# Kernel optimization log

Measured on AMD Instinct MI355X. Metric: run time of the kernel, lower is better.

## Reference

```python
import jax, jax.numpy as jnp
import numpy as np

R = 6
P = 2 * R + 1          # 13, correlation patch size
N = P * P              # 169 displacements
C = 32                 # one-hot label channels
FOUR_LN2 = 4.0 * float(np.log(2.0))


def _extract_windows(x, h, w):
    """Zero-pad by R and extract all PxP shifted views.
    x: (b, c, h, w) -> (b, c, N, h, w), displacement index n = dy*P + dx,
    matching both SpatialCorrelationSampler patch ordering and F.unfold."""
    xp = jnp.pad(x, ((0, 0), (0, 0), (R, R), (R, R)))
    return jnp.stack([xp[:, :, dy:dy + h, dx:dx + w]
                      for dy in range(P) for dx in range(P)], axis=2)


def setup_inputs():
    key = jax.random.key(0)
    k1, k2, k3 = jax.random.split(key, 3)
    feats_r = jax.random.normal(k1, (2, 2, 128, 64, 64), dtype=jnp.float32)
    feats_t = jax.random.normal(k2, (2, 128, 64, 64), dtype=jnp.float32)
    quantized_r = jax.random.randint(k3, (2, 2, 1, 256, 256), 0, C)
    return {"feats_r": feats_r, "feats_t": feats_t, "quantized_r": quantized_r}


def reference(feats_r, feats_t, quantized_r):
    nref, b, c, h, w = feats_r.shape
    hw = h * w

    # ---- local PxP correlation volume per reference (SpatialCorrelationSampler, k=1) ----
    corrs = []
    for i in range(nref):
        win = _extract_windows(feats_r[i], h, w)                       # (b,c,N,h,w)
        corrs.append(jnp.einsum('bchw,bcnhw->bnhw', feats_t, win).reshape(b, N, hw))
    corr = jax.nn.softmax(jnp.concatenate(corrs, axis=1), axis=1)      # (b, nref*N, hw)

    # ---- compact_verify: top-2 + gaussian heatmap refinement ----
    cc = corr.reshape(b, nref, N, hw).transpose(0, 1, 3, 2).reshape(b, nref * hw, N)
    ccd = jax.lax.stop_gradient(cc)                                     # torch uses .detach()
    vals, idx = jax.lax.top_k(ccd, 2)                                   # (b, L, 2)
    wts = jax.nn.softmax(vals, axis=-1)
    ys = (idx // P).astype(jnp.float32)
    xs = (idx % P).astype(jnp.float32)
    grid = jnp.arange(P, dtype=jnp.float32)
    dx = grid[None, None, None, :] - xs[..., None]                      # (b,L,2,P)
    dy = grid[None, None, None, :] - ys[..., None]                      # (b,L,2,P)
    heat = jnp.exp(-FOUR_LN2 * (dx[:, :, :, None, :] ** 2 + dy[:, :, :, :, None] ** 2))  # (b,L,2,P,P) [yy,xx]
    corr_heat = jnp.einsum('blkn,blk->bln', heat.reshape(b, nref * hw, 2, N), wts)
    vmax = jnp.max(vals, axis=-1, keepdims=True)
    corr2 = jnp.where(vmax > 0.1, corr_heat, cc)                        # mask/refine
    corr2 = corr2.reshape(b, nref, hw, N).transpose(0, 1, 3, 2).reshape(b, nref * N, hw)

    # ---- get_out: unfold one-hot reference labels and weighted-sum over window ----
    scale = quantized_r.shape[-2] // h                                  # prep: stride subsample
    ufs = []
    for i in range(nref):
        lab = quantized_r[i, :, 0, ::scale, ::scale]                    # (b,h,w)
        oh = jnp.transpose(jax.nn.one_hot(lab, C, dtype=feats_t.dtype), (0, 3, 1, 2))
        ufs.append(_extract_windows(oh, h, w).reshape(b, C, N, hw))
    image_uf = jnp.concatenate(ufs, axis=2)                             # (b,C,nref*N,hw)
    image_uf = image_uf.at[:, 1:].multiply(1.15)                        # inference boost
    out = jnp.einsum('bnl,bcnl->bcl', corr2, image_uf)
    return out.reshape(b, C, h, w)
```

## Files before the change

### kernel.cpp

```cpp
#include <hip/hip_runtime.h>
#include <math.h>

namespace {

constexpr int RAD  = 6;
constexpr int P    = 13;
constexpr int NWIN = 169;
constexpr int NTOT = 338;
constexpr int NCH  = 128;
constexpr int NCLS = 32;
constexpr int W    = 64;
constexpr int HW   = 4096;
constexpr float FOUR_LN2 = 2.772588722239781f;

constexpr int TX    = 32;
constexpr int CHUNK = 8;
constexpr int PW    = 48;
constexpr int PR    = 13;
constexpr int FRELEMS = CHUNK * PR * PW;
constexpr int NLD   = 20;
constexpr int NCHUNK = NCH / CHUNK;
constexpr int TILE  = TX * NWIN;
constexpr size_t VOLF = (size_t)2 * HW * NTOT;

__device__ __forceinline__ bool better(float va, int ia, float vb, int ib) {
  return (va > vb) || ((va == vb) && (ia < ib));
}

__global__ __launch_bounds__(256, 2) void corr_kernel(
    const float* __restrict__ fr,
    const float* __restrict__ ft,
    float* __restrict__ vol,
    const int* __restrict__ q,
    int* __restrict__ lab) {
  const int blk = blockIdx.x;
  const int t  = threadIdx.x;

  if (blk < 64) {
    const int idx = blk * 256 + t;
    const int i2b = idx >> 12;
    const int rem = idx & 4095;
    const int y2  = rem >> 6;
    const int x2  = rem & 63;
    lab[idx] = q[(size_t)i2b * 65536 + (y2 * 4) * 256 + x2 * 4];
  }

  const int lb = (blk & 7) * 64 + (blk >> 3);
  const int xh = lb & 1;
  const int y  = (lb >> 1) & 63;
  const int bi = lb >> 7;
  const int b  = bi >> 1;
  const int ii = bi & 1;
  const int x0 = xh * TX;
  const int cg = t >> 7;
  const int tl = t & 127;

  __shared__ __align__(16) float smem[2 * FRELEMS];
  __shared__ __align__(16) float ftbuf[2][CHUNK * TX];

  const int xg = tl & 7;
  const int dy = tl >> 3;
  const bool comp = (tl < 104);

  const float* frbase = fr + (size_t)((ii * 2 + b) * NCH) * HW;
  const float* ftp = ft + (size_t)(b * NCH + (t >> 5)) * HW + y * W + x0 + (t & 31);

  int offc[NLD];
  unsigned vmsk = 0u;
  #pragma unroll
  for (int u = 0; u < NLD; ++u) {
    const int e = t + u * 256;
    int o = 0;
    if (e < FRELEMS) {
      const int cc  = e / (PR * PW);
      const int rem = e - cc * (PR * PW);
      const int r   = rem / PW;
      const int xc  = rem - r * PW;
      const int yy  = y + r - RAD;
      const int xx  = x0 - RAD + xc;
      if ((unsigned)yy < 64u && (unsigned)xx < 64u && xc < 44) {
        o = cc * HW + yy * W + xx;
        vmsk |= (1u << u);
      }
    }
    offc[u] = o;
  }

  float acc[13][4];
  #pragma unroll
  for (int dx = 0; dx < 13; ++dx)
    #pragma unroll
    for (int k = 0; k < 4; ++k) acc[dx][k] = 0.f;

  float rg[NLD];
  float rft;

  auto stage_load = [&](int c0) {
    const float* fb = frbase + (size_t)c0 * HW;
    #pragma unroll
    for (int u = 0; u < NLD; ++u) {
      const float v = fb[offc[u]];
      rg[u] = (vmsk & (1u << u)) ? v : 0.f;
    }
    rft = ftp[(size_t)c0 * HW];
  };
  auto stage_write = [&](int s) {
    float* frb = smem + s * FRELEMS;
    #pragma unroll
    for (int u = 0; u < NLD; ++u) {
      const int e = t + u * 256;
      if (e < FRELEMS) frb[e] = rg[u];
    }
    ftbuf[s][t] = rft;
  };

  stage_load(0);
  stage_write(0);
  __syncthreads();

  for (int k = 0; k < NCHUNK; ++k) {
    const int cur = k & 1;
    if (k < NCHUNK - 1) stage_load((k + 1) * CHUNK);
    if (comp) {
      const float* frb = smem + cur * FRELEMS;
      #pragma unroll
      for (int c2 = 0; c2 < 4; ++c2) {
        const int cc = cg * 4 + c2;
        const float* fp = frb + (cc * PR + dy) * PW + xg * 4;
        float w[16];
        #pragma unroll
        for (int j = 0; j < 4; ++j) {
          const float4 q4 = *(const float4*)(fp + 4 * j);
          w[4 * j] = q4.x; w[4 * j + 1] = q4.y; w[4 * j + 2] = q4.z; w[4 * j + 3] = q4.w;
        }
        const float4 tq = *(const float4*)(&ftbuf[cur][cc * TX + xg * 4]);
        const float tqa[4] = {tq.x, tq.y, tq.z, tq.w};
        #pragma unroll
        for (int dx = 0; dx < 13; ++dx)
          #pragma unroll
          for (int kk = 0; kk < 4; ++kk)
            acc[dx][kk] = fmaf(w[dx + kk], tqa[kk], acc[dx][kk]);
      }
    }
    if (k < NCHUNK - 1) stage_write(cur ^ 1);
    __syncthreads();
  }

  if (comp && cg == 1) {
    float* rb = smem + tl * 52;
    #pragma unroll
    for (int dx = 0; dx < 13; ++dx)
      *(float4*)(rb + dx * 4) = make_float4(acc[dx][0], acc[dx][1], acc[dx][2], acc[dx][3]);
  }
  __syncthreads();
  if (comp && cg == 0) {
    const float* rb = smem + tl * 52;
    #pragma unroll
    for (int dx = 0; dx < 13; ++dx) {
      const float4 r = *(const float4*)(rb + dx * 4);
      acc[dx][0] += r.x; acc[dx][1] += r.y; acc[dx][2] += r.z; acc[dx][3] += r.w;
    }
  }
  __syncthreads();
  if (comp && cg == 0) {
    #pragma unroll
    for (int dx = 0; dx < 13; ++dx)
      #pragma unroll
      for (int kk = 0; kk < 4; ++kk)
        smem[(xg * 4 + kk) * NWIN + dy * 13 + dx] = acc[dx][kk];
  }
  __syncthreads();
  {
    float* gb = vol + ((size_t)(b * HW + y * W + x0) * 2 + ii) * NWIN;
    for (int u = 0; u < 22; ++u) {
      const int e = t + u * 256;
      if (e < TILE) {
        const int xl2 = e / NWIN;
        const int mm  = e - xl2 * NWIN;
        gb[(size_t)xl2 * (2 * NWIN) + mm] = smem[e];
      }
    }
  }
}

__global__ __launch_bounds__(256) void post_kernel(
    const float* __restrict__ vol,
    const int*  __restrict__ lab,
    float* __restrict__ out) {
  const int blk  = blockIdx.x;
  const int t    = threadIdx.x;
  const int w    = t >> 6;
  const int lane = t & 63;
  const int pix  = blk * 4 + w;
  const int b = pix >> 12;
  const int y = (pix >> 6) & 63;
  const int x = pix & 63;

  __shared__ float accS[4][NCLS];
  accS[w][lane & 31] = 0.f;

  float vv[6];
  float lmax = -INFINITY;
  const float* vp = vol + (size_t)pix * NTOT;
  #pragma unroll
  for (int k = 0; k < 6; ++k) {
    const int e = lane + 64 * k;
    vv[k] = (e < NTOT) ? vp[e] : -INFINITY;
    lmax = fmaxf(lmax, vv[k]);
  }
  #pragma unroll
  for (int off = 32; off > 0; off >>= 1)
    lmax = fmaxf(lmax, __shfl_xor(lmax, off));

  float p[6];
  float lsum = 0.f;
  #pragma unroll
  for (int k = 0; k < 6; ++k) {
    const int e = lane + 64 * k;
    p[k] = (e < NTOT) ? __expf(vv[k] - lmax) : 0.f;
    lsum += p[k];
  }
  #pragma unroll
  for (int off = 32; off > 0; off >>= 1)
    lsum += __shfl_xor(lsum, off);
  const float rinv = 1.f / lsum;
  #pragma unroll
  for (int k = 0; k < 6; ++k) p[k] *= rinv;

  float a1_0 = -1.f, a2_0 = -1.f, a1_1 = -1.f, a2_1 = -1.f;
  int   j1_0 = 1 << 20, j2_0 = 1 << 20, j1_1 = 1 << 20, j2_1 = 1 << 20;
  #pragma unroll
  for (int k = 0; k < 6; ++k) {
    const int e = lane + 64 * k;
    if (e < NTOT) {
      const int r = (e >= NWIN) ? 1 : 0;
      const int m = e - r * NWIN;
      const float pv = p[k];
      if (r == 0) {
        if (better(pv, m, a1_0, j1_0)) { a2_0 = a1_0; j2_0 = j1_0; a1_0 = pv; j1_0 = m; }
        else if (better(pv, m, a2_0, j2_0)) { a2_0 = pv; j2_0 = m; }
      } else {
        if (better(pv, m, a1_1, j1_1)) { a2_1 = a1_1; j2_1 = j1_1; a1_1 = pv; j1_1 = m; }
        else if (better(pv, m, a2_1, j2_1)) { a2_1 = pv; j2_1 = m; }
      }
    }
  }
  #pragma unroll
  for (int off = 32; off > 0; off >>= 1) {
    {
      const float u1 = __shfl_xor(a1_0, off); const int q1 = __shfl_xor(j1_0, off);
      const float u2 = __shfl_xor(a2_0, off); const int q2 = __shfl_xor(j2_0, off);
      if (better(u1, q1, a1_0, j1_0)) {
        float nv2; int ni2;
        if (better(a1_0, j1_0, u2, q2)) { nv2 = a1_0; ni2 = j1_0; }
        else                            { nv2 = u2;   ni2 = q2; }
        a1_0 = u1; j1_0 = q1; a2_0 = nv2; j2_0 = ni2;
      } else if (better(u1, q1, a2_0, j2_0)) { a2_0 = u1; j2_0 = q1; }
    }
    {
      const float u1 = __shfl_xor(a1_1, off); const int q1 = __shfl_xor(j1_1, off);
      const float u2 = __shfl_xor(a2_1, off); const int q2 = __shfl_xor(j2_1, off);
      if (better(u1, q1, a1_1, j1_1)) {
        float nv2; int ni2;
        if (better(a1_1, j1_1, u2, q2)) { nv2 = a1_1; ni2 = j1_1; }
        else                            { nv2 = u2;   ni2 = q2; }
        a1_1 = u1; j1_1 = q1; a2_1 = nv2; j2_1 = ni2;
      } else if (better(u1, q1, a2_1, j2_1)) { a2_1 = u1; j2_1 = q1; }
    }
  }

  const float e10 = __expf(a1_0), e20 = __expf(a2_0);
  const float rs0 = 1.f / (e10 + e20);
  const float w00 = e10 * rs0, w10 = e20 * rs0;
  const bool  fl0 = (a1_0 > 0.1f);
  const float xs00 = (float)(j1_0 % P), ys00 = (float)(j1_0 / P);
  const float xs10 = (float)(j2_0 % P), ys10 = (float)(j2_0 / P);

  const float e11 = __expf(a1_1), e21 = __expf(a2_1);
  const float rs1 = 1.f / (e11 + e21);
  const float w01 = e11 * rs1, w11 = e21 * rs1;
  const bool  fl1 = (a1_1 > 0.1f);
  const float xs01 = (float)(j1_1 % P), ys01 = (float)(j1_1 / P);
  const float xs11 = (float)(j2_1 % P), ys11 = (float)(j2_1 / P);

  #pragma unroll
  for (int k = 0; k < 6; ++k) {
    const int e = lane + 64 * k;
    if (e < NTOT) {
      const int r  = (e >= NWIN) ? 1 : 0;
      const int m  = e - r * NWIN;
      const int dy = m / P;
      const int dx = m - dy * P;
      const bool  fl = r ? fl1 : fl0;
      float val;
      if (fl) {
        const float wA = r ? w01 : w00, wB = r ? w11 : w10;
        const float xA = r ? xs01 : xs00, yA = r ? ys01 : ys00;
        const float xB = r ? xs11 : xs10, yB = r ? ys11 : ys10;
        const float fdx0 = (float)dx - xA, fdy0 = (float)dy - yA;
        const float fdx1 = (float)dx - xB, fdy1 = (float)dy - yB;
        val = wA * __expf(-FOUR_LN2 * (fdx0 * fdx0 + fdy0 * fdy0))
            + wB * __expf(-FOUR_LN2 * (fdx1 * fdx1 + fdy1 * fdy1));
      } else {
        val = p[k];
      }
      const int yy = y + dy - RAD;
      const int xx = x + dx - RAD;
      if ((unsigned)yy < 64u && (unsigned)xx < 64u) {
        const int cls = lab[(size_t)(r * 2 + b) * 4096 + yy * W + xx];
        atomicAdd(&accS[w][cls], val);
      }
    }
  }
  __syncthreads();

  if (t < 4 * NCLS) {
    const int cls = t >> 2;
    const int j   = t & 3;
    const int x0  = (blk * 4) & 63;
    const float sc = (cls == 0) ? 1.0f : 1.15f;
    out[(size_t)(b * NCLS + cls) * HW + y * W + x0 + j] = accS[j][cls] * sc;
  }
}

}

extern "C" void kernel_launch(void* const* d_in, const int* in_sizes, int n_in,
                              void* d_out, int out_size, void* d_ws, size_t ws_size,
                              hipStream_t stream) {
  const float* fr = (const float*)d_in[0];
  const float* ft = (const float*)d_in[1];
  const int*   q  = (const int*)d_in[2];
  float* out = (float*)d_out;
  float* vol = (float*)d_ws;
  int*   lab = (int*)((char*)d_ws + VOLF * sizeof(float));

  corr_kernel<<<dim3(2 * 2 * 64 * 2), dim3(256), 0, stream>>>(fr, ft, vol, q, lab);
  post_kernel<<<dim3(2 * HW / 4), dim3(256), 0, stream>>>(vol, lab, out);
}
```

Before: 58.77 us.

## Split correlation blocks by displacement-row halves to double grid and occupancy

Each correlation block now handles only 7 or 6 of the 13 vertical displacement rows, which doubles the grid to 2048 blocks and roughly halves shared memory and per-thread accumulators. Threads now compute 2 pixels × 13 dx instead of 4 × 13, and launch bounds are raised to allow 4 blocks per CU. The aim is more parallelism and better latency hiding on a grid that was small. The cost is that feats_t is loaded twice, reference rows overlap partly between halves, and fewer FMAs are done per shared-memory load.

Measured after the change: 59.16 us. About the same (+0.7%).

```diff
diff --git a/kernel.cpp b/kernel.cpp
--- a/kernel.cpp
+++ b/kernel.cpp
@@ -16,18 +16,16 @@
 constexpr int TX    = 32;
 constexpr int CHUNK = 8;
 constexpr int PW    = 48;
-constexpr int PR    = 13;
-constexpr int FRELEMS = CHUNK * PR * PW;
-constexpr int NLD   = 20;
+constexpr int FRMAX = CHUNK * 7 * PW;
+constexpr int NLD   = 11;
 constexpr int NCHUNK = NCH / CHUNK;
-constexpr int TILE  = TX * NWIN;
 constexpr size_t VOLF = (size_t)2 * HW * NTOT;
 
 __device__ __forceinline__ bool better(float va, int ia, float vb, int ib) {
   return (va > vb) || ((va == vb) && (ia < ib));
 }
 
-__global__ __launch_bounds__(256, 2) void corr_kernel(
+__global__ __launch_bounds__(256, 4) void corr_kernel(
     const float* __restrict__ fr,
     const float* __restrict__ ft,
     float* __restrict__ vol,
@@ -45,22 +43,29 @@
     lab[idx] = q[(size_t)i2b * 65536 + (y2 * 4) * 256 + x2 * 4];
   }
 
-  const int lb = (blk & 7) * 64 + (blk >> 3);
-  const int xh = lb & 1;
-  const int y  = (lb >> 1) & 63;
-  const int bi = lb >> 7;
+  const int lb = (blk & 7) * 128 + (blk >> 3);
+  const int h  = lb & 1;
+  const int xh = (lb >> 1) & 1;
+  const int y  = (lb >> 2) & 63;
+  const int bi = lb >> 8;
   const int b  = bi >> 1;
   const int ii = bi & 1;
   const int x0 = xh * TX;
   const int cg = t >> 7;
   const int tl = t & 127;
 
-  __shared__ __align__(16) float smem[2 * FRELEMS];
+  const int RH    = 7 - h;
+  const int yb    = h ? (y + 1) : (y - 6);
+  const int m0    = h * 91;
+  const int frele = CHUNK * RH * PW;
+  const int msz   = RH * P;
+
+  __shared__ __align__(16) float smem[2 * FRMAX];
   __shared__ __align__(16) float ftbuf[2][CHUNK * TX];
 
-  const int xg = tl & 7;
-  const int dy = tl >> 3;
-  const bool comp = (tl < 104);
+  const int xp  = tl & 15;
+  const int dyl = tl >> 4;
+  const bool comp = (dyl < RH);
 
   const float* frbase = fr + (size_t)((ii * 2 + b) * NCH) * HW;
   const float* ftp = ft + (size_t)(b * NCH + (t >> 5)) * HW + y * W + x0 + (t & 31);
@@ -71,12 +76,12 @@
   for (int u = 0; u < NLD; ++u) {
     const int e = t + u * 256;
     int o = 0;
-    if (e < FRELEMS) {
-      const int cc  = e / (PR * PW);
-      const int rem = e - cc * (PR * PW);
+    if (e < frele) {
+      const int cc  = e / (RH * PW);
+      const int rem = e - cc * (RH * PW);
       const int r   = rem / PW;
       const int xc  = rem - r * PW;
-      const int yy  = y + r - RAD;
+      const int yy  = yb + r;
       const int xx  = x0 - RAD + xc;
       if ((unsigned)yy < 64u && (unsigned)xx < 64u && xc < 44) {
         o = cc * HW + yy * W + xx;
@@ -86,11 +91,9 @@
     offc[u] = o;
   }
 
-  float acc[13][4];
-  #pragma unroll
-  for (int dx = 0; dx < 13; ++dx)
-    #pragma unroll
-    for (int k = 0; k < 4; ++k) acc[dx][k] = 0.f;
+  float acc[13][2];
+  #pragma unroll
+  for (int dx = 0; dx < 13; ++dx) { acc[dx][0] = 0.f; acc[dx][1] = 0.f; }
 
   float rg[NLD];
   float rft;
@@ -105,11 +108,11 @@
     rft = ftp[(size_t)c0 * HW];
   };
   auto stage_write = [&](int s) {
-    float* frb = smem + s * FRELEMS;
+    float* frb = smem + s * FRMAX;
     #pragma unroll
     for (int u = 0; u < NLD; ++u) {
       const int e = t + u * 256;
-      if (e < FRELEMS) frb[e] = rg[u];
+      if (e < frele) frb[e] = rg[u];
     }
     ftbuf[s][t] = rft;
   };
@@ -122,24 +125,20 @@
     const int cur = k & 1;
     if (k < NCHUNK - 1) stage_load((k + 1) * CHUNK);
     if (comp) {
-      const float* frb = smem + cur * FRELEMS;
+      const float* frb = smem + cur * FRMAX;
       #pragma unroll
       for (int c2 = 0; c2 < 4; ++c2) {
         const int cc = cg * 4 + c2;
-        const float* fp = frb + (cc * PR + dy) * PW + xg * 4;
-        float w[16];
+        const float* fp = frb + (cc * RH + dyl) * PW + xp * 2;
+        float w[14];
         #pragma unroll
-        for (int j = 0; j < 4; ++j) {
-          const float4 q4 = *(const float4*)(fp + 4 * j);
-          w[4 * j] = q4.x; w[4 * j + 1] = q4.y; w[4 * j + 2] = q4.z; w[4 * j + 3] = q4.w;
+        for (int j = 0; j < 14; ++j) w[j] = fp[j];
+        const float2 tq = *(const float2*)(&ftbuf[cur][cc * TX + xp * 2]);
+        #pragma unroll
+        for (int dx = 0; dx < 13; ++dx) {
+          acc[dx][0] = fmaf(w[dx    ], tq.x, acc[dx][0]);
+          acc[dx][1] = fmaf(w[dx + 1], tq.y, acc[dx][1]);
         }
-        const float4 tq = *(const float4*)(&ftbuf[cur][cc * TX + xg * 4]);
-        const float tqa[4] = {tq.x, tq.y, tq.z, tq.w};
-        #pragma unroll
-        for (int dx = 0; dx < 13; ++dx)
-          #pragma unroll
-          for (int kk = 0; kk < 4; ++kk)
-            acc[dx][kk] = fmaf(w[dx + kk], tqa[kk], acc[dx][kk]);
       }
     }
     if (k < NCHUNK - 1) stage_write(cur ^ 1);
@@ -147,38 +146,38 @@
   }
 
   if (comp && cg == 1) {
-    float* rb = smem + tl * 52;
-    #pragma unroll
-    for (int dx = 0; dx < 13; ++dx)
-      *(float4*)(rb + dx * 4) = make_float4(acc[dx][0], acc[dx][1], acc[dx][2], acc[dx][3]);
+    float* rb = smem + tl * 26;
+    #pragma unroll
+    for (int dx = 0; dx < 13; ++dx) {
+      rb[dx * 2]     = acc[dx][0];
+      rb[dx * 2 + 1] = acc[dx][1];
+    }
   }
   __syncthreads();
   if (comp && cg == 0) {
-    const float* rb = smem + tl * 52;
+    const float* rb = smem + tl * 26;
     #pragma unroll
     for (int dx = 0; dx < 13; ++dx) {
-      const float4 r = *(const float4*)(rb + dx * 4);
-      acc[dx][0] += r.x; acc[dx][1] += r.y; acc[dx][2] += r.z; acc[dx][3] += r.w;
+      acc[dx][0] += rb[dx * 2];
+      acc[dx][1] += rb[dx * 2 + 1];
     }
   }
   __syncthreads();
   if (comp && cg == 0) {
     #pragma unroll
-    for (int dx = 0; dx < 13; ++dx)
-      #pragma unroll
-      for (int kk = 0; kk < 4; ++kk)
-        smem[(xg * 4 + kk) * NWIN + dy * 13 + dx] = acc[dx][kk];
+    for (int dx = 0; dx < 13; ++dx) {
+      smem[(xp * 2    ) * msz + dyl * P + dx] = acc[dx][0];
+      smem[(xp * 2 + 1) * msz + dyl * P + dx] = acc[dx][1];
+    }
   }
   __syncthreads();
   {
-    float* gb = vol + ((size_t)(b * HW + y * W + x0) * 2 + ii) * NWIN;
-    for (int u = 0; u < 22; ++u) {
-      const int e = t + u * 256;
-      if (e < TILE) {
-        const int xl2 = e / NWIN;
-        const int mm  = e - xl2 * NWIN;
-        gb[(size_t)xl2 * (2 * NWIN) + mm] = smem[e];
-      }
+    const int tot = TX * msz;
+    float* gb = vol + ((size_t)(b * HW + y * W + x0) * 2 + ii) * NWIN + m0;
+    for (int e = t; e < tot; e += 256) {
+      const int px = e / msz;
+      const int m  = e - px * msz;
+      gb[(size_t)px * (2 * NWIN) + m] = smem[e];
     }
   }
 }
@@ -335,6 +334,6 @@
   float* vol = (float*)d_ws;
   int*   lab = (int*)((char*)d_ws + VOLF * sizeof(float));
 
-  corr_kernel<<<dim3(2 * 2 * 64 * 2), dim3(256), 0, stream>>>(fr, ft, vol, q, lab);
+  corr_kernel<<<dim3(2 * 2 * 64 * 2 * 2), dim3(256), 0, stream>>>(fr, ft, vol, q, lab);
   post_kernel<<<dim3(2 * HW / 4), dim3(256), 0, stream>>>(vol, lab, out);
 }
```

## Widen correlation register tile to 8 pixels per thread and pack load offsets

Applied to the files above, without the earlier changes.

Each compute thread now accumulates 8 output pixels across all 13 horizontal displacements instead of 4, so only 52 of every 128 threads compute. This raises FMA reuse per shared-memory load. Load offsets are packed two per 32-bit register, and out-of-range loads are skipped outright, with shared memory zeroed once up front instead of writing zeros every stage. This cuts register pressure and memory traffic, but it halves the active compute threads and roughly doubles the accumulator registers, which can hurt latency hiding.

Result: slower. 197.9 us (+236.8%).

```diff
diff --git a/kernel.cpp b/kernel.cpp
--- a/kernel.cpp
+++ b/kernel.cpp
@@ -58,19 +58,19 @@
   __shared__ __align__(16) float smem[2 * FRELEMS];
   __shared__ __align__(16) float ftbuf[2][CHUNK * TX];
 
-  const int xg = tl & 7;
-  const int dy = tl >> 3;
-  const bool comp = (tl < 104);
+  const int xg = tl & 3;
+  const int dy = tl >> 2;
+  const bool comp = (tl < 52);
 
   const float* frbase = fr + (size_t)((ii * 2 + b) * NCH) * HW;
   const float* ftp = ft + (size_t)(b * NCH + (t >> 5)) * HW + y * W + x0 + (t & 31);
 
-  int offc[NLD];
+  unsigned offp[10];
   unsigned vmsk = 0u;
   #pragma unroll
   for (int u = 0; u < NLD; ++u) {
     const int e = t + u * 256;
-    int o = 0;
+    unsigned o = 0;
     if (e < FRELEMS) {
       const int cc  = e / (PR * PW);
       const int rem = e - cc * (PR * PW);
@@ -79,18 +79,20 @@
       const int yy  = y + r - RAD;
       const int xx  = x0 - RAD + xc;
       if ((unsigned)yy < 64u && (unsigned)xx < 64u && xc < 44) {
-        o = cc * HW + yy * W + xx;
+        o = (unsigned)(cc * HW + yy * W + xx);
         vmsk |= (1u << u);
       }
     }
-    offc[u] = o;
-  }
-
-  float acc[13][4];
+    if (u & 1) offp[u >> 1] |= (o << 16); else offp[u >> 1] = o;
+  }
+
+  for (int e = t; e < 2 * FRELEMS; e += 256) smem[e] = 0.f;
+
+  float acc[13][8];
   #pragma unroll
   for (int dx = 0; dx < 13; ++dx)
     #pragma unroll
-    for (int k = 0; k < 4; ++k) acc[dx][k] = 0.f;
+    for (int px = 0; px < 8; ++px) acc[dx][px] = 0.f;
 
   float rg[NLD];
   float rft;
@@ -99,18 +101,18 @@
     const float* fb = frbase + (size_t)c0 * HW;
     #pragma unroll
     for (int u = 0; u < NLD; ++u) {
-      const float v = fb[offc[u]];
-      rg[u] = (vmsk & (1u << u)) ? v : 0.f;
+      if (vmsk & (1u << u)) {
+        const int o = (u & 1) ? (int)(offp[u >> 1] >> 16) : (int)(offp[u >> 1] & 0xffffu);
+        rg[u] = fb[o];
+      }
     }
     rft = ftp[(size_t)c0 * HW];
   };
   auto stage_write = [&](int s) {
     float* frb = smem + s * FRELEMS;
     #pragma unroll
-    for (int u = 0; u < NLD; ++u) {
-      const int e = t + u * 256;
-      if (e < FRELEMS) frb[e] = rg[u];
-    }
+    for (int u = 0; u < NLD; ++u)
+      if (vmsk & (1u << u)) frb[t + u * 256] = rg[u];
     ftbuf[s][t] = rft;
   };
 
@@ -126,20 +128,21 @@
       #pragma unroll
       for (int c2 = 0; c2 < 4; ++c2) {
         const int cc = cg * 4 + c2;
-        const float* fp = frb + (cc * PR + dy) * PW + xg * 4;
-        float w[16];
+        const float* fp = frb + (cc * PR + dy) * PW + xg * 8;
+        float w[20];
         #pragma unroll
-        for (int j = 0; j < 4; ++j) {
+        for (int j = 0; j < 5; ++j) {
           const float4 q4 = *(const float4*)(fp + 4 * j);
           w[4 * j] = q4.x; w[4 * j + 1] = q4.y; w[4 * j + 2] = q4.z; w[4 * j + 3] = q4.w;
         }
-        const float4 tq = *(const float4*)(&ftbuf[cur][cc * TX + xg * 4]);
-        const float tqa[4] = {tq.x, tq.y, tq.z, tq.w};
+        const float4 ta = *(const float4*)(&ftbuf[cur][cc * TX + xg * 8]);
+        const float4 tb = *(const float4*)(&ftbuf[cur][cc * TX + xg * 8 + 4]);
+        const float tq8[8] = {ta.x, ta.y, ta.z, ta.w, tb.x, tb.y, tb.z, tb.w};
         #pragma unroll
         for (int dx = 0; dx < 13; ++dx)
           #pragma unroll
-          for (int kk = 0; kk < 4; ++kk)
-            acc[dx][kk] = fmaf(w[dx + kk], tqa[kk], acc[dx][kk]);
+          for (int px = 0; px < 8; ++px)
+            acc[dx][px] = fmaf(w[dx + px], tq8[px], acc[dx][px]);
       }
     }
     if (k < NCHUNK - 1) stage_write(cur ^ 1);
@@ -147,27 +150,31 @@
   }
 
   if (comp && cg == 1) {
-    float* rb = smem + tl * 52;
-    #pragma unroll
-    for (int dx = 0; dx < 13; ++dx)
-      *(float4*)(rb + dx * 4) = make_float4(acc[dx][0], acc[dx][1], acc[dx][2], acc[dx][3]);
+    float* rb = smem + tl * 104;
+    #pragma unroll
+    for (int dx = 0; dx < 13; ++dx) {
+      *(float4*)(rb + dx * 8)     = make_float4(acc[dx][0], acc[dx][1], acc[dx][2], acc[dx][3]);
+      *(float4*)(rb + dx * 8 + 4) = make_float4(acc[dx][4], acc[dx][5], acc[dx][6], acc[dx][7]);
+    }
   }
   __syncthreads();
   if (comp && cg == 0) {
-    const float* rb = smem + tl * 52;
+    const float* rb = smem + tl * 104;
     #pragma unroll
     for (int dx = 0; dx < 13; ++dx) {
-      const float4 r = *(const float4*)(rb + dx * 4);
-      acc[dx][0] += r.x; acc[dx][1] += r.y; acc[dx][2] += r.z; acc[dx][3] += r.w;
+      const float4 r0 = *(const float4*)(rb + dx * 8);
+      const float4 r1 = *(const float4*)(rb + dx * 8 + 4);
+      acc[dx][0] += r0.x; acc[dx][1] += r0.y; acc[dx][2] += r0.z; acc[dx][3] += r0.w;
+      acc[dx][4] += r1.x; acc[dx][5] += r1.y; acc[dx][6] += r1.z; acc[dx][7] += r1.w;
     }
   }
   __syncthreads();
   if (comp && cg == 0) {
     #pragma unroll
-    for (int dx = 0; dx < 13; ++dx)
+    for (int px = 0; px < 8; ++px)
       #pragma unroll
-      for (int kk = 0; kk < 4; ++kk)
-        smem[(xg * 4 + kk) * NWIN + dy * 13 + dx] = acc[dx][kk];
+      for (int dx = 0; dx < 13; ++dx)
+        smem[(xg * 8 + px) * NWIN + dy * 13 + dx] = acc[dx][px];
   }
   __syncthreads();
   {
```
